# Kernel optimization log

Measured on AMD Instinct MI355X. Metric: run time of the kernel, lower is better.

## Reference

```python
import jax, jax.numpy as jnp
import numpy as np

LN_EPS = 1e-12


def setup_inputs() -> dict:
    key = jax.random.key(0)
    ks = jax.random.split(key, 5)
    E, H, I = 8, 768, 3072
    T = 2048  # tokens per expert (capacity-balanced)
    N = E * T
    return {
        "hidden_states": jax.random.normal(ks[0], (N, H), jnp.float32),
        "w1": jax.random.normal(ks[1], (E, H, I), jnp.float32) * (H ** -0.5),
        "b1": jax.random.normal(ks[2], (E, I), jnp.float32) * 0.02,
        "w2": jax.random.normal(ks[3], (E, I, H), jnp.float32) * (I ** -0.5),
        "b2": jax.random.normal(ks[4], (E, H), jnp.float32) * 0.02,
        "ln_gamma": jnp.ones((H,), jnp.float32),
        "ln_beta": jnp.zeros((H,), jnp.float32),
        "tokens_per_expert": T,
    }


def reference(hidden_states, w1, b1, w2, b2, ln_gamma, ln_beta, tokens_per_expert):
    E = w1.shape[0]
    N, H = hidden_states.shape
    # tokens are pre-sorted by expert; equal capacity per expert -> grouped GEMM
    x = hidden_states.reshape(E, tokens_per_expert, H)  # [E, T, H]
    # dense1 + exact GELU (BERT ACT2FN['gelu'])
    inter = jax.nn.gelu(jnp.einsum("eth,ehi->eti", x, w1) + b1[:, None, :],
                        approximate=False)  # [E, T, I]
    # dense2
    out = jnp.einsum("eti,eih->eth", inter, w2) + b2[:, None, :]  # [E, T, H]
    # dropout is identity in eval mode; residual + LayerNorm
    y = out.reshape(N, H) + hidden_states
    mean = jnp.mean(y, axis=-1, keepdims=True)
    var = jnp.mean(jnp.square(y - mean), axis=-1, keepdims=True)
    return (y - mean) * jax.lax.rsqrt(var + LN_EPS) * ln_gamma + ln_beta
```

## Files before the change

### kernel.cpp

```cpp
#include <hip/hip_runtime.h>
#include <hip/hip_bf16.h>
#include <math.h>

#define E_   8
#define H_   768
#define I_   3072
#define T_   2048
#define NTOK (E_ * T_)

typedef __attribute__((ext_vector_type(8))) short bf16x8;
typedef __attribute__((ext_vector_type(4))) float f32x4;

typedef __attribute__((address_space(3))) void lds_void;
typedef const __attribute__((address_space(1))) void gl_void;

__device__ __forceinline__ void gload16(const void* g, void* l) {
  __builtin_amdgcn_global_load_lds((gl_void*)g, (lds_void*)l, 16, 0, 0);
}

#define FENCE() asm volatile("" ::: "memory")
#define BAR()                         \
  do {                                \
    FENCE();                          \
    __builtin_amdgcn_s_barrier();     \
    FENCE();                          \
  } while (0)
#define VMWAIT(n) asm volatile("s_waitcnt vmcnt(" #n ")" ::: "memory")

#define MFMA16(a, b, c) __builtin_amdgcn_mfma_f32_16x16x32_bf16(a, b, c, 0, 0, 0)

__device__ __forceinline__ float gelu_fast(float v) {
  float inner = v * fmaf(v * v, 0.044715f, 1.0f);
  float e = __builtin_amdgcn_exp2f(inner * -2.3022082f);
  return v * __builtin_amdgcn_rcpf(1.0f + e);
}

#define CVT_BLOCKS 12288
#define WT_BLOCKS  4608

__global__ __launch_bounds__(256) void prep_kernel(
    const float* __restrict__ x, __hip_bfloat16* __restrict__ x_bf,
    const float* __restrict__ w1, __hip_bfloat16* __restrict__ w1t,
    const float* __restrict__ w2, __hip_bfloat16* __restrict__ w2t) {
  __shared__ __hip_bfloat16 tile[64][66];
  int b = blockIdx.x;

  if (b < CVT_BLOCKS) {
    int i = (b * 256 + threadIdx.x) * 4;
    float4 v = *(const float4*)(x + i);
    __align__(8) __hip_bfloat16 t[4];
    t[0] = __float2bfloat16(v.x);
    t[1] = __float2bfloat16(v.y);
    t[2] = __float2bfloat16(v.z);
    t[3] = __float2bfloat16(v.w);
    *(ushort4*)(x_bf + i) = *(const ushort4*)t;
    return;
  }

  const float* src;
  __hip_bfloat16* dst;
  int R, C, c0, r0;
  if (b < CVT_BLOCKS + WT_BLOCKS) {
    int t = b - CVT_BLOCKS;
    int e = t / 576, rem = t % 576;
    R = H_; C = I_;
    c0 = (rem % 48) * 64;
    r0 = (rem / 48) * 64;
    src = w1 + (size_t)e * R * C;
    dst = w1t + (size_t)e * R * C;
  } else {
    int t = b - (CVT_BLOCKS + WT_BLOCKS);
    int e = t / 576, rem = t % 576;
    R = I_; C = H_;
    c0 = (rem % 12) * 64;
    r0 = (rem / 12) * 64;
    src = w2 + (size_t)e * R * C;
    dst = w2t + (size_t)e * R * C;
  }

  int tx = threadIdx.x & 31;
  int ty = threadIdx.x >> 5;
#pragma unroll
  for (int r = ty; r < 64; r += 8) {
    float2 v = *(const float2*)&src[(size_t)(r0 + r) * C + c0 + 2 * tx];
    __hip_bfloat16 b0 = __float2bfloat16(v.x);
    __hip_bfloat16 b1 = __float2bfloat16(v.y);
    ushort2 w;
    w.x = *(const ushort*)&b0;
    w.y = *(const ushort*)&b1;
    *(ushort2*)&tile[r][2 * tx] = w;
  }
  __syncthreads();
#pragma unroll
  for (int rr = ty; rr < 64; rr += 8) {
    ushort2 v;
    v.x = *(const ushort*)&tile[2 * tx][rr];
    v.y = *(const ushort*)&tile[2 * tx + 1][rr];
    *(ushort2*)&dst[(size_t)(c0 + rr) * R + r0 + 2 * tx] = v;
  }
}

template <int K, int N, int BN, bool GELU>
__global__ __launch_bounds__(512, 2) void gemm2p_kernel(
    const __hip_bfloat16* __restrict__ A,
    const __hip_bfloat16* __restrict__ B,
    const float* __restrict__ bias,
    __hip_bfloat16* __restrict__ out) {
  constexpr int MT = T_ / 256;
  constexpr int NT = N / BN;
  constexpr int KT = K / 64;
  constexpr int NF = BN / 64;
  constexpr int WCW = BN / 4;
  constexpr int BPASS = BN / 64;

  __shared__ __hip_bfloat16 sA[2][2][128][64];
  __shared__ __hip_bfloat16 sB[2][BN][64];

  int nwg = gridDim.x;
  int b0  = blockIdx.x;
  int bid = (b0 & 7) * (nwg >> 3) + (b0 >> 3);

  int e   = bid / (MT * NT);
  int rr_ = bid % (MT * NT);
  int bm  = rr_ / NT;
  int bn  = rr_ % NT;

  const __hip_bfloat16* Ae = A + (size_t)e * T_ * K + (size_t)bm * 256 * K;
  const __hip_bfloat16* Be = B + (size_t)e * N  * K + (size_t)bn * BN * K;

  int tid  = threadIdx.x;
  int lane = tid & 63;
  int wid  = tid >> 6;
  int wr   = wid >> 2;
  int wc   = wid & 3;
  int l15  = lane & 15;
  int l16h = lane >> 4;

  int i0 = tid, i1 = 512 + tid;
  int lr0 = i0 >> 3, c80 = i0 & 7, cg0 = c80 ^ (lr0 & 7);
  int lr1 = i1 >> 3, c81 = i1 & 7, cg1 = c81 ^ (lr1 & 7);
  int rA0 = ((lr0 >> 6) << 7) | (lr0 & 63);
  int rA1 = ((lr1 >> 6) << 7) | (lr1 & 63);
  const size_t oA0 = (size_t)rA0 * K + cg0 * 8;
  const size_t oA1 = (size_t)rA1 * K + cg1 * 8;
  const size_t HOFF = (size_t)64 * K;
  size_t oB[BPASS];
  int    dB[BPASS];
#pragma unroll
  for (int q = 0; q < BPASS; ++q) {
    int idx = q * 512 + tid;
    int lr = idx >> 3, c8 = idx & 7;
    int cg = c8 ^ (lr & 7);
    oB[q] = (size_t)lr * K + cg * 8;
    dB[q] = lr * 64 + c8 * 8;
  }

  auto stageA = [&](int buf, int h, int kt) {
    const __hip_bfloat16* g = Ae + (size_t)kt * 64 + (size_t)h * HOFF;
    gload16(g + oA0, &sA[buf][h][lr0][c80 * 8]);
    gload16(g + oA1, &sA[buf][h][lr1][c81 * 8]);
  };
  auto stageB = [&](int buf, int kt) {
    const __hip_bfloat16* g = Be + (size_t)kt * 64;
    __hip_bfloat16* l = &sB[buf][0][0];
#pragma unroll
    for (int q = 0; q < BPASS; ++q) gload16(g + oB[q], l + dB[q]);
  };

  int laBase = wr * 64 + l15;
  int lbBase = wc * WCW + l15;
  int s7   = l15 & 7;
  int cgr0 = ((0 | l16h) ^ s7) * 8;
  int cgr1 = ((4 | l16h) ^ s7) * 8;

  f32x4 acc[8][NF] = {};
  bf16x8 af[4][2], bfv[NF][2];

  stageA(0, 0, 0);
  stageB(0, 0);
  stageA(0, 1, 0);

  auto ktile = [&](int kt, int p, bool pf) {
    VMWAIT(2);
    BAR();
#pragma unroll
    for (int mf = 0; mf < 4; ++mf) {
      int la = laBase + mf * 16;
      af[mf][0] = *(const bf16x8*)&sA[p][0][la][cgr0];
      af[mf][1] = *(const bf16x8*)&sA[p][0][la][cgr1];
    }
#pragma unroll
    for (int nf = 0; nf < NF; ++nf) {
      int lb = lbBase + nf * 16;
      bfv[nf][0] = *(const bf16x8*)&sB[p][lb][cgr0];
      bfv[nf][1] = *(const bf16x8*)&sB[p][lb][cgr1];
    }
    if (pf) {
      stageA(p ^ 1, 0, kt + 1);
      stageB(p ^ 1, kt + 1);
    }
    __builtin_amdgcn_s_setprio(1);
#pragma unroll
    for (int mf = 0; mf < 4; ++mf)
#pragma unroll
      for (int nf = 0; nf < NF; ++nf) {
        acc[mf][nf] = MFMA16(af[mf][0], bfv[nf][0], acc[mf][nf]);
        acc[mf][nf] = MFMA16(af[mf][1], bfv[nf][1], acc[mf][nf]);
      }
    __builtin_amdgcn_s_setprio(0);
    if (pf) {
      if constexpr (BN == 256) { VMWAIT(6); } else { VMWAIT(5); }
    } else {
      VMWAIT(0);
    }
    BAR();
#pragma unroll
    for (int mf = 0; mf < 4; ++mf) {
      int la = laBase + mf * 16;
      af[mf][0] = *(const bf16x8*)&sA[p][1][la][cgr0];
      af[mf][1] = *(const bf16x8*)&sA[p][1][la][cgr1];
    }
    if (pf) stageA(p ^ 1, 1, kt + 1);
    __builtin_amdgcn_s_setprio(1);
#pragma unroll
    for (int mf = 0; mf < 4; ++mf)
#pragma unroll
      for (int nf = 0; nf < NF; ++nf) {
        acc[4 + mf][nf] = MFMA16(af[mf][0], bfv[nf][0], acc[4 + mf][nf]);
        acc[4 + mf][nf] = MFMA16(af[mf][1], bfv[nf][1], acc[4 + mf][nf]);
      }
    __builtin_amdgcn_s_setprio(0);
  };

  int p = 0;
  for (int kt = 0; kt < KT - 1; ++kt) {
    ktile(kt, p, true);
    p ^= 1;
  }
  ktile(KT - 1, p, false);

  const float* be = bias + (size_t)e * N + bn * BN;
  __hip_bfloat16* oe =
      out + (size_t)e * T_ * N + (size_t)(bm * 256) * N + bn * BN;
  int r4 = l16h * 4;
#pragma unroll
  for (int mi = 0; mi < 8; ++mi) {
    int mh = mi >> 2, mf = mi & 3;
    int rowb = wr * 128 + mh * 64 + mf * 16 + r4;
#pragma unroll
    for (int nf = 0; nf < NF; ++nf) {
      int cc   = wc * WCW + nf * 16 + l15;
      float bv = be[cc];
#pragma unroll
      for (int r = 0; r < 4; ++r) {
        float v = acc[mi][nf][r] + bv;
        if (GELU) v = gelu_fast(v);
        oe[(size_t)(rowb + r) * N + cc] = __float2bfloat16(v);
      }
    }
  }
}

__global__ __launch_bounds__(384) void ln_kernel(
    const __hip_bfloat16* __restrict__ yraw,
    const __hip_bfloat16* __restrict__ xbf,
    const float* __restrict__ gamma, const float* __restrict__ beta,
    float* __restrict__ out) {
  int row  = blockIdx.x;
  int tid  = threadIdx.x;
  int lane = tid & 63, wid = tid >> 6;
  int c    = tid * 2;
  const __hip_bfloat16* yr = yraw + (size_t)row * H_;
  const __hip_bfloat16* xr = xbf + (size_t)row * H_;

  ushort2 ya = *(const ushort2*)&yr[c];
  ushort2 xa = *(const ushort2*)&xr[c];
  __hip_bfloat16 t;
  float v0, v1;
  *(ushort*)&t = ya.x; v0 = __bfloat162float(t);
  *(ushort*)&t = xa.x; v0 += __bfloat162float(t);
  *(ushort*)&t = ya.y; v1 = __bfloat162float(t);
  *(ushort*)&t = xa.y; v1 += __bfloat162float(t);

  float s = v0 + v1, s2 = v0 * v0 + v1 * v1;
#pragma unroll
  for (int o = 32; o > 0; o >>= 1) {
    s  += __shfl_down(s, o);
    s2 += __shfl_down(s2, o);
  }
  __shared__ float ls[6], ls2[6];
  if (lane == 0) { ls[wid] = s; ls2[wid] = s2; }
  __syncthreads();
  float tot  = ls[0] + ls[1] + ls[2] + ls[3] + ls[4] + ls[5];
  float tot2 = ls2[0] + ls2[1] + ls2[2] + ls2[3] + ls2[4] + ls2[5];
  float mean = tot * (1.0f / 768.0f);
  float var  = tot2 * (1.0f / 768.0f) - mean * mean;
  float inv  = rsqrtf(var + 1e-12f);
  float2 g = *(const float2*)&gamma[c];
  float2 b = *(const float2*)&beta[c];
  float2 o2;
  o2.x = (v0 - mean) * inv * g.x + b.x;
  o2.y = (v1 - mean) * inv * g.y + b.y;
  *(float2*)&out[(size_t)row * H_ + c] = o2;
}

extern "C" void kernel_launch(void* const* d_in, const int* in_sizes, int n_in,
                              void* d_out, int out_size, void* d_ws,
                              size_t ws_size, hipStream_t stream) {
  const float* x     = (const float*)d_in[0];
  const float* w1    = (const float*)d_in[1];
  const float* b1    = (const float*)d_in[2];
  const float* w2    = (const float*)d_in[3];
  const float* b2    = (const float*)d_in[4];
  const float* gamma = (const float*)d_in[5];
  const float* beta  = (const float*)d_in[6];
  float* out = (float*)d_out;

  char* ws = (char*)d_ws;
  __hip_bfloat16* w1t   = (__hip_bfloat16*)(ws);
  __hip_bfloat16* w2t   = (__hip_bfloat16*)(ws + 37748736);
  __hip_bfloat16* x_bf  = (__hip_bfloat16*)(ws + 75497472);
  __hip_bfloat16* inter = (__hip_bfloat16*)(ws + 100663296);
  __hip_bfloat16* yraw  = (__hip_bfloat16*)(ws);

  prep_kernel<<<CVT_BLOCKS + 2 * WT_BLOCKS, 256, 0, stream>>>(
      x, x_bf, w1, w1t, w2, w2t);
  gemm2p_kernel<H_, I_, 256, true>
      <<<E_ * (T_ / 256) * (I_ / 256), 512, 0, stream>>>(x_bf, w1t, b1, inter);
  gemm2p_kernel<I_, H_, 192, false>
      <<<E_ * (T_ / 256) * (H_ / 192), 512, 0, stream>>>(inter, w2t, b2, yraw);
  ln_kernel<<<NTOK, 384, 0, stream>>>(yraw, x_bf, gamma, beta, out);
}
```

Measured before the change: 238.5 us.

## Use 12-wave 768-thread GEMM blocks with 192-wide N tiles for both GEMMs

Both grouped GEMMs now run with 768 threads (12 waves arranged 2x6), each wave owning a 128x32 output sub-tile. Only the first 512 threads load A, and all threads load B with two loads each, so the wait counts differ per thread group. The first GEMM moves from BN=256 to BN=192 to share the same kernel. The aim is more waves per CU and fewer accumulator registers per wave to hide latency better. The cost is less MFMA work per loaded fragment, a more complex per-thread wait scheme, and launch bounds that may force register spilling.

New measurement: 239.1 us (median of 2 runs). About the same (+0.2%).

```diff
diff --git a/kernel.cpp b/kernel.cpp
--- a/kernel.cpp
+++ b/kernel.cpp
@@ -100,18 +100,16 @@
   }
 }
 
-template <int K, int N, int BN, bool GELU>
-__global__ __launch_bounds__(512, 2) void gemm2p_kernel(
+template <int K, int N, bool GELU>
+__global__ __launch_bounds__(768, 3) void gemm12w_kernel(
     const __hip_bfloat16* __restrict__ A,
     const __hip_bfloat16* __restrict__ B,
     const float* __restrict__ bias,
     __hip_bfloat16* __restrict__ out) {
+  constexpr int BN = 192;
   constexpr int MT = T_ / 256;
   constexpr int NT = N / BN;
   constexpr int KT = K / 64;
-  constexpr int NF = BN / 64;
-  constexpr int WCW = BN / 4;
-  constexpr int BPASS = BN / 64;
 
   __shared__ __hip_bfloat16 sA[2][2][128][64];
   __shared__ __hip_bfloat16 sB[2][BN][64];
@@ -131,10 +129,11 @@
   int tid  = threadIdx.x;
   int lane = tid & 63;
   int wid  = tid >> 6;
-  int wr   = wid >> 2;
-  int wc   = wid & 3;
+  int wr   = wid / 6;
+  int wc   = wid % 6;
   int l15  = lane & 15;
   int l16h = lane >> 4;
+  bool isX = (tid < 512);
 
   int i0 = tid, i1 = 512 + tid;
   int lr0 = i0 >> 3, c80 = i0 & 7, cg0 = c80 ^ (lr0 & 7);
@@ -144,11 +143,11 @@
   const size_t oA0 = (size_t)rA0 * K + cg0 * 8;
   const size_t oA1 = (size_t)rA1 * K + cg1 * 8;
   const size_t HOFF = (size_t)64 * K;
-  size_t oB[BPASS];
-  int    dB[BPASS];
-#pragma unroll
-  for (int q = 0; q < BPASS; ++q) {
-    int idx = q * 512 + tid;
+  size_t oB[2];
+  int    dB[2];
+#pragma unroll
+  for (int q = 0; q < 2; ++q) {
+    int idx = q * 768 + tid;
     int lr = idx >> 3, c8 = idx & 7;
     int cg = c8 ^ (lr & 7);
     oB[q] = (size_t)lr * K + cg * 8;
@@ -156,32 +155,34 @@
   }
 
   auto stageA = [&](int buf, int h, int kt) {
-    const __hip_bfloat16* g = Ae + (size_t)kt * 64 + (size_t)h * HOFF;
-    gload16(g + oA0, &sA[buf][h][lr0][c80 * 8]);
-    gload16(g + oA1, &sA[buf][h][lr1][c81 * 8]);
+    if (isX) {
+      const __hip_bfloat16* g = Ae + (size_t)kt * 64 + (size_t)h * HOFF;
+      gload16(g + oA0, &sA[buf][h][lr0][c80 * 8]);
+      gload16(g + oA1, &sA[buf][h][lr1][c81 * 8]);
+    }
   };
   auto stageB = [&](int buf, int kt) {
     const __hip_bfloat16* g = Be + (size_t)kt * 64;
     __hip_bfloat16* l = &sB[buf][0][0];
-#pragma unroll
-    for (int q = 0; q < BPASS; ++q) gload16(g + oB[q], l + dB[q]);
+    gload16(g + oB[0], l + dB[0]);
+    gload16(g + oB[1], l + dB[1]);
   };
 
   int laBase = wr * 64 + l15;
-  int lbBase = wc * WCW + l15;
+  int lbBase = wc * 32 + l15;
   int s7   = l15 & 7;
   int cgr0 = ((0 | l16h) ^ s7) * 8;
   int cgr1 = ((4 | l16h) ^ s7) * 8;
 
-  f32x4 acc[8][NF] = {};
-  bf16x8 af[4][2], bfv[NF][2];
+  f32x4 acc[8][2] = {};
+  bf16x8 af[4][2], bfv[2][2];
 
   stageA(0, 0, 0);
   stageB(0, 0);
   stageA(0, 1, 0);
 
   auto ktile = [&](int kt, int p, bool pf) {
-    VMWAIT(2);
+    if (isX) { VMWAIT(2); } else { VMWAIT(0); }
     BAR();
 #pragma unroll
     for (int mf = 0; mf < 4; ++mf) {
@@ -190,7 +191,7 @@
       af[mf][1] = *(const bf16x8*)&sA[p][0][la][cgr1];
     }
 #pragma unroll
-    for (int nf = 0; nf < NF; ++nf) {
+    for (int nf = 0; nf < 2; ++nf) {
       int lb = lbBase + nf * 16;
       bfv[nf][0] = *(const bf16x8*)&sB[p][lb][cgr0];
       bfv[nf][1] = *(const bf16x8*)&sB[p][lb][cgr1];
@@ -203,15 +204,15 @@
 #pragma unroll
     for (int mf = 0; mf < 4; ++mf)
 #pragma unroll
-      for (int nf = 0; nf < NF; ++nf) {
+      for (int nf = 0; nf < 2; ++nf) {
         acc[mf][nf] = MFMA16(af[mf][0], bfv[nf][0], acc[mf][nf]);
         acc[mf][nf] = MFMA16(af[mf][1], bfv[nf][1], acc[mf][nf]);
       }
     __builtin_amdgcn_s_setprio(0);
     if (pf) {
-      if constexpr (BN == 256) { VMWAIT(6); } else { VMWAIT(5); }
+      if (isX) { VMWAIT(4); }
     } else {
-      VMWAIT(0);
+      if (isX) { VMWAIT(0); }
     }
     BAR();
 #pragma unroll
@@ -225,7 +226,7 @@
 #pragma unroll
     for (int mf = 0; mf < 4; ++mf)
 #pragma unroll
-      for (int nf = 0; nf < NF; ++nf) {
+      for (int nf = 0; nf < 2; ++nf) {
         acc[4 + mf][nf] = MFMA16(af[mf][0], bfv[nf][0], acc[4 + mf][nf]);
         acc[4 + mf][nf] = MFMA16(af[mf][1], bfv[nf][1], acc[4 + mf][nf]);
       }
@@ -248,8 +249,8 @@
     int mh = mi >> 2, mf = mi & 3;
     int rowb = wr * 128 + mh * 64 + mf * 16 + r4;
 #pragma unroll
-    for (int nf = 0; nf < NF; ++nf) {
-      int cc   = wc * WCW + nf * 16 + l15;
+    for (int nf = 0; nf < 2; ++nf) {
+      int cc   = wc * 32 + nf * 16 + l15;
       float bv = be[cc];
 #pragma unroll
       for (int r = 0; r < 4; ++r) {
@@ -325,9 +326,9 @@
 
   prep_kernel<<<CVT_BLOCKS + 2 * WT_BLOCKS, 256, 0, stream>>>(
       x, x_bf, w1, w1t, w2, w2t);
-  gemm2p_kernel<H_, I_, 256, true>
-      <<<E_ * (T_ / 256) * (I_ / 256), 512, 0, stream>>>(x_bf, w1t, b1, inter);
-  gemm2p_kernel<I_, H_, 192, false>
-      <<<E_ * (T_ / 256) * (H_ / 192), 512, 0, stream>>>(inter, w2t, b2, yraw);
+  gemm12w_kernel<H_, I_, true>
+      <<<E_ * (T_ / 256) * (I_ / 192), 768, 0, stream>>>(x_bf, w1t, b1, inter);
+  gemm12w_kernel<I_, H_, false>
+      <<<E_ * (T_ / 256) * (H_ / 192), 768, 0, stream>>>(inter, w2t, b2, yraw);
   ln_kernel<<<NTOK, 384, 0, stream>>>(yraw, x_bf, gamma, beta, out);
 }
```
